# Optimization experiments

Hardware: AMD Instinct MI355X
Metric: run time of the kernel (lower is better)

Reference implementation:

```python
import jax, jax.numpy as jnp
import numpy as np

P = 16; RES = 224; D = 768; L = 12; H = 12; OUT = 512
NP1 = NP2 = RES // P          # 14x14 patches
NTOK = NP1 * NP2 + 1          # 197 tokens (cls + patches)
STD = 5.0                     # gaussian_std for naclip
EPS = 1e-5


def _ln(x, w, b):
    x32 = x.astype(jnp.float32)
    m = x32.mean(-1, keepdims=True)
    v = ((x32 - m) ** 2).mean(-1, keepdims=True)
    return (((x32 - m) * jax.lax.rsqrt(v + EPS)) * w + b).astype(x.dtype)


def _quick_gelu(x):
    return x * jax.nn.sigmoid(1.702 * x)


def _gaussian_addition():
    # VisionTransformer.gaussian_window + get_attention_addition, done analytically:
    # addition[i*NP2+j, k*NP2+l] = window[k-i+NP1-1, l-j+NP2-1]
    w1, w2 = 2 * NP1 - 1, 2 * NP2 - 1
    c = 1.0 / (STD * np.sqrt(2.0))
    k1 = (-(w1 - 1) / 2.0 + np.arange(w1)) * c
    k2 = (-(w2 - 1) / 2.0 + np.arange(w2)) * c
    window = np.exp(-(k1[:, None] ** 2 + k2[None, :] ** 2))
    r = np.arange(NP1)[None, :] - np.arange(NP1)[:, None] + (NP1 - 1)  # [i,k]
    cc = np.arange(NP2)[None, :] - np.arange(NP2)[:, None] + (NP2 - 1)  # [j,l]
    A = window[r[:, None, :, None], cc[None, :, None, :]]  # (NP1,NP2,NP1,NP2)
    A = A.reshape(NP1 * NP2, NP1 * NP2)
    full = np.zeros((NTOK, NTOK), dtype=np.float32)
    full[1:, 1:] = A  # zero row/col for cls token
    return jnp.asarray(full)


def _mha_vanilla(x, wi, bi, wo, bo):
    B, N, _ = x.shape
    hd = D // H
    qkv = x @ wi.T + bi                      # [B,N,3D]
    q, k, v = jnp.split(qkv, 3, axis=-1)
    q = q.reshape(B, N, H, hd); k = k.reshape(B, N, H, hd); v = v.reshape(B, N, H, hd)
    a = jnp.einsum('bqhd,bkhd->bhqk', q, k) * (hd ** -0.5)
    a = jax.nn.softmax(a, axis=-1)
    o = jnp.einsum('bhqk,bkhd->bqhd', a, v).reshape(B, N, D)
    return o @ wo.T + bo


def _mha_naclip(x, wi, bi, wo, bo, addition):
    B, N, _ = x.shape
    hd = D // H
    qkv = x @ wi.T + bi
    _, k, v = jnp.split(qkv, 3, axis=-1)
    k = k.reshape(B, N, H, hd); v = v.reshape(B, N, H, hd)
    a = jnp.einsum('bqhd,bkhd->bhqk', k, k) * (hd ** -0.5) + addition[None, None]
    a = jax.nn.softmax(a, axis=-1)
    o = jnp.einsum('bhqk,bkhd->bqhd', a, v).reshape(B, N, D)
    return o @ wo.T + bo


def _mlp(x, fw, fb, pw, pb):
    return _quick_gelu(x @ fw.T + fb) @ pw.T + pb


def setup_inputs() -> dict:
    key = jax.random.key(0)
    ks = jax.random.split(key, 16)
    s = D ** -0.5
    rn = lambda k, shape, sc=0.02: jax.random.normal(k, shape, jnp.float32) * sc
    return {
        'x': jax.random.normal(ks[0], (32, 3, RES, RES), jnp.float32),
        'conv1_w': rn(ks[1], (D, 3, P, P)),
        'class_embedding': rn(ks[2], (D,), s),
        'pos_embedding': rn(ks[3], (NTOK, D), s),
        'ln_pre_w': jnp.ones((D,)), 'ln_pre_b': jnp.zeros((D,)),
        'in_proj_w': rn(ks[4], (L, 3 * D, D)), 'in_proj_b': rn(ks[5], (L, 3 * D)),
        'out_proj_w': rn(ks[6], (L, D, D)), 'out_proj_b': rn(ks[7], (L, D)),
        'ln1_w': jnp.ones((L, D)), 'ln1_b': jnp.zeros((L, D)),
        'ln2_w': jnp.ones((L, D)), 'ln2_b': jnp.zeros((L, D)),
        'fc_w': rn(ks[8], (L, 4 * D, D)), 'fc_b': rn(ks[9], (L, 4 * D)),
        'cproj_w': rn(ks[10], (L, D, 4 * D)), 'cproj_b': rn(ks[11], (L, D)),
        'ln_post_w': jnp.ones((D,)), 'ln_post_b': jnp.zeros((D,)),
        'proj': rn(ks[12], (D, OUT), s),
    }


def reference(x, conv1_w, class_embedding, pos_embedding, ln_pre_w, ln_pre_b,
              in_proj_w, in_proj_b, out_proj_w, out_proj_b, ln1_w, ln1_b,
              ln2_w, ln2_b, fc_w, fc_b, cproj_w, cproj_b, ln_post_w, ln_post_b, proj):
    B = x.shape[0]
    # patch embed
    h = jax.lax.conv_general_dilated(x, conv1_w, (P, P), 'VALID',
                                     dimension_numbers=('NCHW', 'OIHW', 'NCHW'))
    h = h.reshape(B, D, NP1 * NP2).transpose(0, 2, 1)           # [B,196,D]
    cls = jnp.broadcast_to(class_embedding, (B, 1, D))
    h = jnp.concatenate([cls, h], axis=1) + pos_embedding        # [B,197,D]
    h = _ln(h, ln_pre_w, ln_pre_b)
    addition = _gaussian_addition()
    # first L-1 blocks: vanilla attention
    for i in range(L - 1):
        h = h + _mha_vanilla(_ln(h, ln1_w[i], ln1_b[i]), in_proj_w[i], in_proj_b[i],
                             out_proj_w[i], out_proj_b[i])
        h = h + _mlp(_ln(h, ln2_w[i], ln2_b[i]), fc_w[i], fc_b[i], cproj_w[i], cproj_b[i])
    # last block: naclip key-key attention with gaussian addition (arch='vanilla')
    i = L - 1
    reduced = _mha_naclip(_ln(h, ln1_w[i], ln1_b[i]), in_proj_w[i], in_proj_b[i],
                          out_proj_w[i], out_proj_b[i], addition)
    final = h + reduced
    final = final + _mlp(_ln(final, ln2_w[i], ln2_b[i]), fc_w[i], fc_b[i], cproj_w[i], cproj_b[i])
    return _ln(final, ln_post_w, ln_post_b) @ proj               # [B,197,OUT]
```

## Files before the change

### kernel.cpp

```cpp
#include <hip/hip_runtime.h>
#include <hip/hip_bf16.h>
#include <math.h>

#define BATCH 32
#define NTOK  197
#define NPATCH 196
#define DMODEL 768
#define NLAYER 12
#define NHEAD 12
#define HDIM  64
#define ROWS  (BATCH*NTOK)
#define CROWS (BATCH*NPATCH)
#define DFF   3072
#define DQKV  2304
#define DOUT  512
#define NBH   (BATCH*NHEAD)

#define WOFF_IN   ((size_t)0)
#define WOFF_OUT  ((size_t)(DQKV*DMODEL))
#define WOFF_FC   (WOFF_OUT + (size_t)(DMODEL*DMODEL))
#define WOFF_CP   (WOFF_FC + (size_t)(DFF*DMODEL))
#define WTOT      (WOFF_CP + (size_t)(DMODEL*DFF))

#define WS_H    ((size_t)0)
#define WS_QKVB (WS_H + (size_t)ROWS*DMODEL)
#define WS_GB   (WS_QKVB + (size_t)ROWS*DQKV/2)
#define WS_TB   (WS_GB + (size_t)ROWS*DFF/2)
#define WS_WL   (WS_TB + (size_t)ROWS*DMODEL/2)
#define WS_PTS  (WS_WL + WTOT/2)
#define WS_ADD  (WS_PTS + (size_t)DOUT*DMODEL/2)

typedef unsigned short ushort_t;
typedef __attribute__((ext_vector_type(8))) short bf16x8;
typedef __attribute__((ext_vector_type(4))) float f32x4;

__device__ inline ushort_t bf16rn(float x) {
    uint32_t u = __builtin_bit_cast(uint32_t, x);
    uint32_t r = (u + 0x7FFFu + ((u >> 16) & 1u)) >> 16;
    return (ushort_t)r;
}

#define GLL(src, dst) __builtin_amdgcn_global_load_lds( \
    (const __attribute__((address_space(1))) void*)(src), \
    (__attribute__((address_space(3))) void*)(dst), 16, 0, 0)


__global__ void im2col_bf16_k(const float* __restrict__ x, ushort_t* __restrict__ out) {
    int idx = blockIdx.x * 256 + threadIdx.x;
    if (idx >= CROWS * DMODEL / 4) return;
    int r  = idx / (DMODEL / 4);
    int k4 = (idx - r * (DMODEL / 4)) * 4;
    int b = r / NPATCH, p = r - b * NPATCH;
    int py = p / 14, px = p - py * 14;
    int c = k4 >> 8, rem = k4 & 255, i = rem >> 4, j = rem & 15;
    const float* xp = x + (((size_t)(b * 3 + c) * 224) + py * 16 + i) * 224 + px * 16 + j;
    float4 v = *(const float4*)xp;
    ushort4 hv = {bf16rn(v.x), bf16rn(v.y), bf16rn(v.z), bf16rn(v.w)};
    *(ushort4*)(out + (size_t)r * DMODEL + k4) = hv;
}

__global__ void cvt_w_k(const float* __restrict__ W, ushort_t* __restrict__ out, int NK) {
    int idx = (blockIdx.x * 256 + threadIdx.x) * 4;
    if (idx >= NK) return;
    float4 v = *(const float4*)(W + idx);
    ushort4 hv = {bf16rn(v.x), bf16rn(v.y), bf16rn(v.z), bf16rn(v.w)};
    *(ushort4*)(out + idx) = hv;
}

__global__ void cvt_layer_k(const float* __restrict__ inW, const float* __restrict__ outW,
                            const float* __restrict__ fcW, const float* __restrict__ cpW,
                            ushort_t* __restrict__ wl) {
    size_t idx = ((size_t)blockIdx.x * 256 + threadIdx.x) * 4;
    if (idx >= WTOT) return;
    const float* src; size_t off;
    if (idx < WOFF_OUT)      { src = inW;  off = idx; }
    else if (idx < WOFF_FC)  { src = outW; off = idx - WOFF_OUT; }
    else if (idx < WOFF_CP)  { src = fcW;  off = idx - WOFF_FC; }
    else                     { src = cpW;  off = idx - WOFF_CP; }
    float4 v = *(const float4*)(src + off);
    ushort4 hv = {bf16rn(v.x), bf16rn(v.y), bf16rn(v.z), bf16rn(v.w)};
    *(ushort4*)(wl + idx) = hv;
}

__global__ void cvt_pT_k(const float* __restrict__ proj, ushort_t* __restrict__ out) {
    int idx = blockIdx.x * 256 + threadIdx.x;
    if (idx >= DOUT * DMODEL) return;
    int n = idx / DMODEL, k = idx - n * DMODEL;
    out[(size_t)n * DMODEL + k] = bf16rn(proj[(size_t)k * DOUT + n]);
}

__global__ void embed_k(const float* __restrict__ conv, const float* __restrict__ cls,
                        const float* __restrict__ pos, float* __restrict__ h) {
    int idx = blockIdx.x * 256 + threadIdx.x;
    if (idx >= ROWS * DMODEL) return;
    int r = idx / DMODEL, d = idx - r * DMODEL;
    int b = r / NTOK, tok = r - b * NTOK;
    float v = (tok == 0) ? cls[d] : conv[((size_t)(b * NPATCH + tok - 1)) * DMODEL + d];
    h[idx] = v + pos[(size_t)tok * DMODEL + d];
}

__global__ void gauss_k(float* __restrict__ add) {
    int idx = blockIdx.x * 256 + threadIdx.x;
    if (idx >= NTOK * NTOK) return;
    int i = idx / NTOK, j = idx - i * NTOK;
    float v = 0.f;
    if (i > 0 && j > 0) {
        int p = i - 1, q = j - 1;
        int di = q / 14 - p / 14;
        int dj = q % 14 - p % 14;
        v = expf(-(float)(di * di + dj * dj) * 0.02f);
    }
    add[idx] = v;
}

__global__ __launch_bounds__(256) void ln768_k(const float* __restrict__ in, float* __restrict__ out,
                                               const float* __restrict__ w, const float* __restrict__ b) {
    int row = blockIdx.x, tid = threadIdx.x;
    const float* x = in + (size_t)row * DMODEL;
    float v0 = x[tid], v1 = x[tid + 256], v2 = x[tid + 512];
    float s = v0 + v1 + v2;
    float s2 = v0 * v0 + v1 * v1 + v2 * v2;
    for (int o = 32; o > 0; o >>= 1) { s += __shfl_down(s, o); s2 += __shfl_down(s2, o); }
    __shared__ float red[8];
    int wid = tid >> 6;
    if ((tid & 63) == 0) { red[wid] = s; red[4 + wid] = s2; }
    __syncthreads();
    s  = red[0] + red[1] + red[2] + red[3];
    s2 = red[4] + red[5] + red[6] + red[7];
    float mean = s * (1.0f / 768.0f);
    float var  = s2 * (1.0f / 768.0f) - mean * mean;
    float rinv = rsqrtf(var + 1e-5f);
    float* o_ = out + (size_t)row * DMODEL;
    o_[tid]       = (v0 - mean) * rinv * w[tid]       + b[tid];
    o_[tid + 256] = (v1 - mean) * rinv * w[tid + 256] + b[tid + 256];
    o_[tid + 512] = (v2 - mean) * rinv * w[tid + 512] + b[tid + 512];
}

__global__ __launch_bounds__(256) void ln768_bf16_k(const float* __restrict__ in, ushort_t* __restrict__ out,
                                                    const float* __restrict__ w, const float* __restrict__ b) {
    int row = blockIdx.x, tid = threadIdx.x;
    const float* x = in + (size_t)row * DMODEL;
    float v0 = x[tid], v1 = x[tid + 256], v2 = x[tid + 512];
    float s = v0 + v1 + v2;
    float s2 = v0 * v0 + v1 * v1 + v2 * v2;
    for (int o = 32; o > 0; o >>= 1) { s += __shfl_down(s, o); s2 += __shfl_down(s2, o); }
    __shared__ float red[8];
    int wid = tid >> 6;
    if ((tid & 63) == 0) { red[wid] = s; red[4 + wid] = s2; }
    __syncthreads();
    s  = red[0] + red[1] + red[2] + red[3];
    s2 = red[4] + red[5] + red[6] + red[7];
    float mean = s * (1.0f / 768.0f);
    float var  = s2 * (1.0f / 768.0f) - mean * mean;
    float rinv = rsqrtf(var + 1e-5f);
    ushort_t* o_ = out + (size_t)row * DMODEL;
    o_[tid]       = bf16rn((v0 - mean) * rinv * w[tid]       + b[tid]);
    o_[tid + 256] = bf16rn((v1 - mean) * rinv * w[tid + 256] + b[tid + 256]);
    o_[tid + 512] = bf16rn((v2 - mean) * rinv * w[tid + 512] + b[tid + 512]);
}

__global__ __launch_bounds__(256) void gemm_mfma_k(
    const ushort_t* __restrict__ A, const ushort_t* __restrict__ W,
    const float* __restrict__ bias, float* __restrict__ C, ushort_t* __restrict__ OS,
    int M, int N, int K, int mode)
{
    __shared__ ushort_t As[3][128][32];
    __shared__ ushort_t Bs[3][128][32];
    int tid = threadIdx.x;
    int lane = tid & 63;
    int wave = tid >> 6;
    int wm = wave >> 1, wn = wave & 1;
    int m0 = blockIdx.x * 128, n0 = blockIdx.y * 128;

    int klen = K / gridDim.z;
    int kbeg = blockIdx.z * klen;
    int nt = klen / 32;

    f32x4 acc[4][4];
    #pragma unroll
    for (int i = 0; i < 4; ++i)
        #pragma unroll
        for (int j = 0; j < 4; ++j)
            acc[i][j] = (f32x4){0.f, 0.f, 0.f, 0.f};

    int srow = tid >> 2;
    int skq  = (((tid & 3) ^ ((tid >> 3) & 3)) * 8);
    int ar0 = m0 + srow;      if (ar0 > M - 1) ar0 = M - 1;
    int ar1 = m0 + srow + 64; if (ar1 > M - 1) ar1 = M - 1;
    const ushort_t* Ap0 = A + (size_t)ar0 * K + kbeg + skq;
    const ushort_t* Ap1 = A + (size_t)ar1 * K + kbeg + skq;
    const ushort_t* Wp0 = W + (size_t)(n0 + srow) * K + kbeg + skq;
    const ushort_t* Wp1 = W + (size_t)(n0 + srow + 64) * K + kbeg + skq;
    char* ldsA = (char*)As + tid * 16;
    char* ldsB = (char*)Bs + tid * 16;

    int fr = lane & 15, fq = lane >> 4;
    int rsl = (fq ^ ((fr >> 1) & 3)) * 8;

    #define STAGE(buf_, ko_) do {                         \
        GLL(Ap0 + (ko_), ldsA + (buf_) * 8192);           \
        GLL(Ap1 + (ko_), ldsA + (buf_) * 8192 + 4096);    \
        GLL(Wp0 + (ko_), ldsB + (buf_) * 8192);           \
        GLL(Wp1 + (ko_), ldsB + (buf_) * 8192 + 4096);    \
    } while (0)

    STAGE(0, 0);
    STAGE(1, 32);

    for (int t = 0; t < nt; ++t) {
        int cur = t % 3;
        if (t + 2 < nt) {
            STAGE((t + 2) % 3, (size_t)(t + 2) * 32);
            asm volatile("s_waitcnt vmcnt(8)\n\ts_barrier" ::: "memory");
        } else if (t + 1 < nt) {
            asm volatile("s_waitcnt vmcnt(4)\n\ts_barrier" ::: "memory");
        } else {
            asm volatile("s_waitcnt vmcnt(0)\n\ts_barrier" ::: "memory");
        }
        bf16x8 a[4], b[4];
        #pragma unroll
        for (int fm = 0; fm < 4; ++fm)
            a[fm] = *(const bf16x8*)&As[cur][wm * 64 + fm * 16 + fr][rsl];
        #pragma unroll
        for (int fn = 0; fn < 4; ++fn)
            b[fn] = *(const bf16x8*)&Bs[cur][wn * 64 + fn * 16 + fr][rsl];
        #pragma unroll
        for (int fm = 0; fm < 4; ++fm)
            #pragma unroll
            for (int fn = 0; fn < 4; ++fn)
                acc[fm][fn] = __builtin_amdgcn_mfma_f32_16x16x32_bf16(a[fm], b[fn], acc[fm][fn], 0, 0, 0);
        asm volatile("s_barrier" ::: "memory");
    }
    #undef STAGE

    #pragma unroll
    for (int fn = 0; fn < 4; ++fn) {
        int ccol = n0 + wn * 64 + fn * 16 + fr;
        float bv = bias ? bias[ccol] : 0.f;
        if (mode == 3 && blockIdx.z != 0) bv = 0.f;
        #pragma unroll
        for (int fm = 0; fm < 4; ++fm) {
            int crow0 = m0 + wm * 64 + fm * 16 + fq * 4;
            #pragma unroll
            for (int j = 0; j < 4; ++j) {
                int row = crow0 + j;
                if (row < M) {
                    float v = acc[fm][fn][j] + bv;
                    if (mode == 0) {
                        C[(size_t)row * N + ccol] = v;
                    } else if (mode == 3) {
                        atomicAdd(&C[(size_t)row * N + ccol], v);
                    } else if (mode == 4) {
                        OS[(size_t)row * N + ccol] = bf16rn(v);
                    } else {
                        v = v / (1.0f + expf(-1.702f * v));
                        OS[(size_t)row * N + ccol] = bf16rn(v);
                    }
                }
            }
        }
    }
}

__global__ __launch_bounds__(512, 4) void attn_fused_k(
    const ushort_t* __restrict__ qkvb, ushort_t* __restrict__ out,
    const float* __restrict__ addition, int qoff)
{
    __shared__ ushort_t Ks[208][72];
    __shared__ ushort_t Vt[64][232];
    __shared__ ushort_t Pb[8][2][16][40];
    int tid = threadIdx.x;
    int bh = blockIdx.x;
    int b = bh / NHEAD, hh = bh - b * NHEAD;
    const ushort_t* base = qkvb + (size_t)b * NTOK * DQKV + hh * HDIM;

    int lane = tid & 63, wave = tid >> 6;
    int fr = lane & 15, fq = lane >> 4;
    int nq = (wave + 8 < 13) ? 2 : 1;

    bf16x8 qf[2][2];
    #pragma unroll
    for (int t = 0; t < 2; ++t) {
        if (t < nq) {
            int qrow = (wave + t * 8) * 16 + fr; if (qrow > NTOK - 1) qrow = NTOK - 1;
            const ushort_t* qp = base + (size_t)qrow * DQKV + qoff + fq * 8;
            qf[t][0] = *(const bf16x8*)qp;
            qf[t][1] = *(const bf16x8*)(qp + 32);
        }
    }

    {
        int tt = tid >> 4, dq = tid & 15;
        #pragma unroll
        for (int pass = 0; pass < 7; ++pass) {
            int t = pass * 32 + tt;
            if (t < 208) {
                ushort4 kv = {0, 0, 0, 0}, vv = {0, 0, 0, 0};
                if (t < NTOK) {
                    kv = *(const ushort4*)(base + (size_t)t * DQKV + DMODEL + dq * 4);
                    vv = *(const ushort4*)(base + (size_t)t * DQKV + 2 * DMODEL + dq * 4);
                }
                *(ushort4*)&Ks[t][dq * 4] = kv;
                Vt[dq * 4 + 0][t] = vv.x;
                Vt[dq * 4 + 1][t] = vv.y;
                Vt[dq * 4 + 2][t] = vv.z;
                Vt[dq * 4 + 3][t] = vv.w;
            }
        }
        for (int z = tid; z < 64 * 24; z += 512) Vt[z / 24][208 + z % 24] = 0;
    }
    __syncthreads();

    for (int t = 0; t < nq; ++t) {
        int qt = wave + t * 8;
        int i0 = qt * 16;
        int irow = i0 + fr; if (irow > NTOK - 1) irow = NTOK - 1;

        f32x4 s[13];
        #pragma unroll
        for (int jt = 0; jt < 13; ++jt) {
            bf16x8 k0 = *(const bf16x8*)&Ks[jt * 16 + fr][fq * 8];
            bf16x8 k1 = *(const bf16x8*)&Ks[jt * 16 + fr][32 + fq * 8];
            f32x4 a = {0.f, 0.f, 0.f, 0.f};
            a = __builtin_amdgcn_mfma_f32_16x16x32_bf16(k0, qf[t][0], a, 0, 0, 0);
            a = __builtin_amdgcn_mfma_f32_16x16x32_bf16(k1, qf[t][1], a, 0, 0, 0);
            s[jt] = a;
        }

        float mx = -1e30f;
        #pragma unroll
        for (int jt = 0; jt < 13; ++jt) {
            int jb = jt * 16 + fq * 4;
            #pragma unroll
            for (int jj = 0; jj < 4; ++jj) {
                int j = jb + jj;
                float v = s[jt][jj] * 0.125f;
                if (addition) v += addition[irow * NTOK + (j < NTOK ? j : NTOK - 1)];
                if (j >= NTOK) v = -1e30f;
                s[jt][jj] = v;
                mx = fmaxf(mx, v);
            }
        }
        mx = fmaxf(mx, __shfl_xor(mx, 16));
        mx = fmaxf(mx, __shfl_xor(mx, 32));
        float sum = 0.f;
        #pragma unroll
        for (int jt = 0; jt < 13; ++jt)
            #pragma unroll
            for (int jj = 0; jj < 4; ++jj) {
                float e = __expf(s[jt][jj] - mx);
                s[jt][jj] = e;
                sum += e;
            }
        sum += __shfl_xor(sum, 16);
        sum += __shfl_xor(sum, 32);
        float inv = 1.0f / sum;

        f32x4 o4[4];
        #pragma unroll
        for (int dt = 0; dt < 4; ++dt) o4[dt] = (f32x4){0.f, 0.f, 0.f, 0.f};

        #define WRITE_P(st_, buf_) do {                                              \
            int jA = 2 * (st_), jB = jA + 1;                                         \
            ushort4 wa = {bf16rn(s[jA][0] * inv), bf16rn(s[jA][1] * inv),            \
                          bf16rn(s[jA][2] * inv), bf16rn(s[jA][3] * inv)};           \
            ushort4 wb = {0, 0, 0, 0};                                               \
            if (jB < 13) wb = (ushort4){bf16rn(s[jB][0] * inv), bf16rn(s[jB][1] * inv), \
                                        bf16rn(s[jB][2] * inv), bf16rn(s[jB][3] * inv)}; \
            *(ushort4*)&Pb[wave][buf_][fr][fq * 4] = wa;                             \
            *(ushort4*)&Pb[wave][buf_][fr][16 + fq * 4] = wb;                        \
        } while (0)

        WRITE_P(0, 0);
        for (int st = 0; st < 7; ++st) {
            asm volatile("s_waitcnt lgkmcnt(0)" ::: "memory");
            bf16x8 pa = *(const bf16x8*)&Pb[wave][st & 1][fr][fq * 8];
            bf16x8 vf0 = *(const bf16x8*)&Vt[0 * 16 + fr][st * 32 + fq * 8];
            bf16x8 vf1 = *(const bf16x8*)&Vt[1 * 16 + fr][st * 32 + fq * 8];
            bf16x8 vf2 = *(const bf16x8*)&Vt[2 * 16 + fr][st * 32 + fq * 8];
            bf16x8 vf3 = *(const bf16x8*)&Vt[3 * 16 + fr][st * 32 + fq * 8];
            if (st < 6) WRITE_P(st + 1, (st + 1) & 1);
            o4[0] = __builtin_amdgcn_mfma_f32_16x16x32_bf16(pa, vf0, o4[0], 0, 0, 0);
            o4[1] = __builtin_amdgcn_mfma_f32_16x16x32_bf16(pa, vf1, o4[1], 0, 0, 0);
            o4[2] = __builtin_amdgcn_mfma_f32_16x16x32_bf16(pa, vf2, o4[2], 0, 0, 0);
            o4[3] = __builtin_amdgcn_mfma_f32_16x16x32_bf16(pa, vf3, o4[3], 0, 0, 0);
        }
        #undef WRITE_P

        #pragma unroll
        for (int jj = 0; jj < 4; ++jj) {
            int ir = i0 + fq * 4 + jj;
            if (ir < NTOK) {
                ushort_t* op = out + ((size_t)(b * NTOK + ir)) * DMODEL + hh * HDIM + fr;
                #pragma unroll
                for (int dt = 0; dt < 4; ++dt)
                    op[dt * 16] = bf16rn(o4[dt][jj]);
            }
        }
    }
}

extern "C" void kernel_launch(void* const* d_in, const int* in_sizes, int n_in,
                              void* d_out, int out_size, void* d_ws, size_t ws_size,
                              hipStream_t stream) {
    const float* x        = (const float*)d_in[0];
    const float* conv1_w  = (const float*)d_in[1];
    const float* cls      = (const float*)d_in[2];
    const float* pos      = (const float*)d_in[3];
    const float* ln_pre_w = (const float*)d_in[4];
    const float* ln_pre_b = (const float*)d_in[5];
    const float* in_proj_w  = (const float*)d_in[6];
    const float* in_proj_b  = (const float*)d_in[7];
    const float* out_proj_w = (const float*)d_in[8];
    const float* out_proj_b = (const float*)d_in[9];
    const float* ln1_w = (const float*)d_in[10];
    const float* ln1_b = (const float*)d_in[11];
    const float* ln2_w = (const float*)d_in[12];
    const float* ln2_b = (const float*)d_in[13];
    const float* fc_w  = (const float*)d_in[14];
    const float* fc_b  = (const float*)d_in[15];
    const float* cproj_w = (const float*)d_in[16];
    const float* cproj_b = (const float*)d_in[17];
    const float* ln_post_w = (const float*)d_in[18];
    const float* ln_post_b = (const float*)d_in[19];
    const float* proj = (const float*)d_in[20];
    float* out = (float*)d_out;

    float* ws   = (float*)d_ws;
    float* h    = ws + WS_H;
    float* ctmp = ws + WS_QKVB;
    ushort_t* qkvb = (ushort_t*)(ws + WS_QKVB);
    ushort_t* gb   = (ushort_t*)(ws + WS_GB);
    ushort_t* tb   = (ushort_t*)(ws + WS_TB);
    ushort_t* wl   = (ushort_t*)(ws + WS_WL);
    ushort_t* pTs  = (ushort_t*)(ws + WS_PTS);
    float* add  = ws + WS_ADD;

    im2col_bf16_k<<<(CROWS * DMODEL / 4 + 255) / 256, 256, 0, stream>>>(x, tb);
    cvt_w_k<<<(DMODEL * DMODEL / 4 + 255) / 256, 256, 0, stream>>>(conv1_w, wl, DMODEL * DMODEL);
    gemm_mfma_k<<<dim3((CROWS + 127) / 128, DMODEL / 128), 256, 0, stream>>>(
        tb, wl, nullptr, ctmp, nullptr, CROWS, DMODEL, DMODEL, 0);
    embed_k<<<(ROWS * DMODEL + 255) / 256, 256, 0, stream>>>(ctmp, cls, pos, h);
    ln768_k<<<ROWS, 256, 0, stream>>>(h, h, ln_pre_w, ln_pre_b);
    gauss_k<<<(NTOK * NTOK + 255) / 256, 256, 0, stream>>>(add);
    cvt_pT_k<<<(DOUT * DMODEL + 255) / 256, 256, 0, stream>>>(proj, pTs);

    const int GY = (ROWS + 127) / 128;
    for (int l = 0; l < NLAYER; ++l) {
        cvt_layer_k<<<(int)(WTOT / 4 / 256), 256, 0, stream>>>(
            in_proj_w + (size_t)l * DQKV * DMODEL, out_proj_w + (size_t)l * DMODEL * DMODEL,
            fc_w + (size_t)l * DFF * DMODEL, cproj_w + (size_t)l * DMODEL * DFF, wl);
        ln768_bf16_k<<<ROWS, 256, 0, stream>>>(h, tb, ln1_w + l * DMODEL, ln1_b + l * DMODEL);
        gemm_mfma_k<<<dim3(GY, DQKV / 128), 256, 0, stream>>>(
            tb, wl + WOFF_IN, in_proj_b + (size_t)l * DQKV, nullptr, qkvb, ROWS, DQKV, DMODEL, 4);
        bool nac = (l == NLAYER - 1);
        attn_fused_k<<<NBH, 512, 0, stream>>>(qkvb, tb, nac ? add : nullptr, nac ? DMODEL : 0);
        gemm_mfma_k<<<dim3(GY, DMODEL / 128, 2), 256, 0, stream>>>(
            tb, wl + WOFF_OUT, out_proj_b + (size_t)l * DMODEL, h, nullptr, ROWS, DMODEL, DMODEL, 3);
        ln768_bf16_k<<<ROWS, 256, 0, stream>>>(h, tb, ln2_w + l * DMODEL, ln2_b + l * DMODEL);
        gemm_mfma_k<<<dim3(GY, DFF / 128), 256, 0, stream>>>(
            tb, wl + WOFF_FC, fc_b + (size_t)l * DFF, nullptr, gb, ROWS, DFF, DMODEL, 1);
        gemm_mfma_k<<<dim3(GY, DMODEL / 128, 2), 256, 0, stream>>>(
            gb, wl + WOFF_CP, cproj_b + (size_t)l * DMODEL, h, nullptr, ROWS, DMODEL, DFF, 3);
    }

    ln768_bf16_k<<<ROWS, 256, 0, stream>>>(h, tb, ln_post_w, ln_post_b);
    gemm_mfma_k<<<dim3(GY, DOUT / 128), 256, 0, stream>>>(
        tb, pTs, nullptr, out, nullptr, ROWS, DOUT, DMODEL, 0);
}
```

Before: 3.525 ms.

## Merge GEMM K-loop barriers and split attention query tiles across two blocks

The GEMM main loop now uses one barrier per iteration instead of two. The prefetch of stage t+2 is issued after the current tile's fragments are read from LDS, so the trailing barrier can go, while loads still overlap the MFMA work. Separately, the attention kernel launches twice as many blocks (grid y=2), with each wave handling at most one query tile instead of looping over two. This gives more parallelism and better balance, but each block must now reload and re-transpose K and V into LDS.

```diff
diff --git a/kernel.cpp b/kernel.cpp
--- a/kernel.cpp
+++ b/kernel.cpp
@@ -205,18 +205,16 @@
     } while (0)
 
     STAGE(0, 0);
-    STAGE(1, 32);
+    if (nt > 1) STAGE(1, 32);
 
     for (int t = 0; t < nt; ++t) {
         int cur = t % 3;
-        if (t + 2 < nt) {
-            STAGE((t + 2) % 3, (size_t)(t + 2) * 32);
-            asm volatile("s_waitcnt vmcnt(8)\n\ts_barrier" ::: "memory");
-        } else if (t + 1 < nt) {
-            asm volatile("s_waitcnt vmcnt(4)\n\ts_barrier" ::: "memory");
+        if (t + 1 < nt) {
+            asm volatile("s_waitcnt vmcnt(4)" ::: "memory");
         } else {
-            asm volatile("s_waitcnt vmcnt(0)\n\ts_barrier" ::: "memory");
-        }
+            asm volatile("s_waitcnt vmcnt(0)" ::: "memory");
+        }
+        __builtin_amdgcn_s_barrier();
         bf16x8 a[4], b[4];
         #pragma unroll
         for (int fm = 0; fm < 4; ++fm)
@@ -224,12 +222,12 @@
         #pragma unroll
         for (int fn = 0; fn < 4; ++fn)
             b[fn] = *(const bf16x8*)&Bs[cur][wn * 64 + fn * 16 + fr][rsl];
+        if (t + 2 < nt) STAGE((t + 2) % 3, (size_t)(t + 2) * 32);
         #pragma unroll
         for (int fm = 0; fm < 4; ++fm)
             #pragma unroll
             for (int fn = 0; fn < 4; ++fn)
                 acc[fm][fn] = __builtin_amdgcn_mfma_f32_16x16x32_bf16(a[fm], b[fn], acc[fm][fn], 0, 0, 0);
-        asm volatile("s_barrier" ::: "memory");
     }
     #undef STAGE
 
@@ -276,17 +274,14 @@
 
     int lane = tid & 63, wave = tid >> 6;
     int fr = lane & 15, fq = lane >> 4;
-    int nq = (wave + 8 < 13) ? 2 : 1;
-
-    bf16x8 qf[2][2];
-    #pragma unroll
-    for (int t = 0; t < 2; ++t) {
-        if (t < nq) {
-            int qrow = (wave + t * 8) * 16 + fr; if (qrow > NTOK - 1) qrow = NTOK - 1;
-            const ushort_t* qp = base + (size_t)qrow * DQKV + qoff + fq * 8;
-            qf[t][0] = *(const bf16x8*)qp;
-            qf[t][1] = *(const bf16x8*)(qp + 32);
-        }
+    int qt = blockIdx.y * 8 + wave;
+
+    bf16x8 qf0, qf1;
+    if (qt < 13) {
+        int qrow = qt * 16 + fr; if (qrow > NTOK - 1) qrow = NTOK - 1;
+        const ushort_t* qp = base + (size_t)qrow * DQKV + qoff + fq * 8;
+        qf0 = *(const bf16x8*)qp;
+        qf1 = *(const bf16x8*)(qp + 32);
     }
 
     {
@@ -311,8 +306,7 @@
     }
     __syncthreads();
 
-    for (int t = 0; t < nq; ++t) {
-        int qt = wave + t * 8;
+    if (qt < 13) {
         int i0 = qt * 16;
         int irow = i0 + fr; if (irow > NTOK - 1) irow = NTOK - 1;
 
@@ -322,8 +316,8 @@
             bf16x8 k0 = *(const bf16x8*)&Ks[jt * 16 + fr][fq * 8];
             bf16x8 k1 = *(const bf16x8*)&Ks[jt * 16 + fr][32 + fq * 8];
             f32x4 a = {0.f, 0.f, 0.f, 0.f};
-            a = __builtin_amdgcn_mfma_f32_16x16x32_bf16(k0, qf[t][0], a, 0, 0, 0);
-            a = __builtin_amdgcn_mfma_f32_16x16x32_bf16(k1, qf[t][1], a, 0, 0, 0);
+            a = __builtin_amdgcn_mfma_f32_16x16x32_bf16(k0, qf0, a, 0, 0, 0);
+            a = __builtin_amdgcn_mfma_f32_16x16x32_bf16(k1, qf1, a, 0, 0, 0);
             s[jt] = a;
         }
 
@@ -454,7 +448,7 @@
         gemm_mfma_k<<<dim3(GY, DQKV / 128), 256, 0, stream>>>(
             tb, wl + WOFF_IN, in_proj_b + (size_t)l * DQKV, nullptr, qkvb, ROWS, DQKV, DMODEL, 4);
         bool nac = (l == NLAYER - 1);
-        attn_fused_k<<<NBH, 512, 0, stream>>>(qkvb, tb, nac ? add : nullptr, nac ? DMODEL : 0);
+        attn_fused_k<<<dim3(NBH, 2), 512, 0, stream>>>(qkvb, tb, nac ? add : nullptr, nac ? DMODEL : 0);
         gemm_mfma_k<<<dim3(GY, DMODEL / 128, 2), 256, 0, stream>>>(
             tb, wl + WOFF_OUT, out_proj_b + (size_t)l * DMODEL, h, nullptr, ROWS, DMODEL, DMODEL, 3);
         ln768_bf16_k<<<ROWS, 256, 0, stream>>>(h, tb, ln2_w + l * DMODEL, ln2_b + l * DMODEL);
```

After: 3.267 ms. 7.3% less time.
